# Performance work log

Hardware: AMD Instinct MI355X
Metric: run time of the kernel (lower is better)

Reference implementation:

```python
import jax, jax.numpy as jnp
import numpy as np

B, L, LA, LL = 256, 512, 8, 64
V, D, P, HOPS = 100000, 300, 3, 3


def setup_inputs() -> dict:
    key = jax.random.key(0)
    ks = jax.random.split(key, 18)
    sc = 0.05
    return {
        "text":   jax.random.randint(ks[0], (B, L),  0, V),
        "aspect": jax.random.randint(ks[1], (B, LA), 0, V),
        "left":   jax.random.randint(ks[2], (B, LL), 0, V),
        # pretrained embedding table
        "embed": jax.random.normal(ks[3], (V, D), jnp.float32) * 0.1,
        # all Linear weights stored as [in, out] (y = x @ W + b)
        "Wx": jax.random.normal(ks[4], (D, D), jnp.float32) * sc,   # x_linear (no bias)
        "Ws": jax.random.normal(ks[5], (D, D), jnp.float32) * sc,   # s_linear (no bias)
        "Wk": jax.random.normal(ks[6], (D, D), jnp.float32) * sc,   # attention w_k
        "bk": jnp.zeros((D,), jnp.float32),
        "Wq": jax.random.normal(ks[7], (D, D), jnp.float32) * sc,   # attention w_q
        "bq": jnp.zeros((D,), jnp.float32),
        "w_mlp": jax.random.normal(ks[8], (2 * D,), jnp.float32) * sc,  # attention mlp score vector
        "Wproj": jax.random.normal(ks[9], (D, D), jnp.float32) * sc,    # attention proj
        "bproj": jnp.zeros((D,), jnp.float32),
        "Wm": jax.random.normal(ks[10], (D, D), jnp.float32) * sc,  # mlp
        "bm": jnp.zeros((D,), jnp.float32),
        "Wd": jax.random.normal(ks[11], (D, P), jnp.float32) * sc,  # dense
        "bd": jnp.zeros((P,), jnp.float32),
    }


def _forward(text, aspect, left, embed, Wx, Ws, Wk, bk, Wq, bq, w_mlp,
             Wproj, bproj, Wm, bm, Wd, bd):
    f32 = jnp.float32
    left_len = (left != 0).sum(-1)    # (B,)
    mem_len = (text != 0).sum(-1)     # (B,)
    asp_len = (aspect != 0).sum(-1)   # (B,)
    mem_len_f = mem_len.astype(f32)

    # aspect mean-pooled query (sum over all positions / nonzero count, as in torch code)
    asp_e = embed[aspect].sum(1) / asp_len.astype(f32)[:, None]   # (B, D)
    x = asp_e[:, None, :]                                         # (B, 1, D)

    memory = embed[text]                                          # (B, L, D)
    v_s = (memory.sum(1) / mem_len_f[:, None])[:, None, :]        # (B, 1, D)

    # SqueezeEmbedding (zero padding) + vectorized locationed_memory decay
    idx = jnp.arange(L, dtype=f32)[None, :]                       # (1, L)
    start = (left_len - asp_len).astype(f32)[:, None]             # aspect_start
    end = left_len.astype(f32)[:, None]                           # aspect_end
    l = jnp.where(idx < start, start - idx,
                  jnp.where(idx <= end, 0.0, idx - end))          # (B, L)
    w = 1.0 - l / mem_len_f[:, None]
    w = jnp.where(idx < mem_len_f[:, None], w, 0.0)               # zero padded positions
    memory = memory * w[:, :, None]                               # (B, L, D)

    for _ in range(HOPS):
        x = x @ Wx                                                # (B, 1, D)
        s = v_s @ Ws                                              # computed but unused (faithful)
        # Attention(score_function='mlp', n_head=1, hidden=D)
        kx = memory @ Wk + bk                                     # (B, L, D)
        qx = x @ Wq + bq                                          # (B, 1, D)
        # tanh(cat(kx, qx) @ w_mlp) == tanh(kx@w1 + qx@w2)
        score = jnp.tanh(kx @ w_mlp[:D] + qx @ w_mlp[D:])         # (B, L)
        score = jax.nn.softmax(score, axis=-1)
        v_ts = jnp.einsum('bl,bld->bd', score, kx)[:, None, :]    # (B, 1, D)
        v_ts = v_ts @ Wproj + bproj

    v_ns = (v_ts + v_s).reshape(text.shape[0], -1)                # (B, D)
    v_ms = jnp.tanh(v_ns @ Wm + bm)
    out = jax.nn.softmax(v_ms @ Wd + bd, axis=-1)                 # (B, P)
    return out


def reference(text, aspect, left, embed, Wx, Ws, Wk, bk, Wq, bq, w_mlp,
              Wproj, bproj, Wm, bm, Wd, bd):
    return _forward(text, aspect, left, embed, Wx, Ws, Wk, bk, Wq, bq,
                    w_mlp, Wproj, bproj, Wm, bm, Wd, bd)
```

## Files before the change

kernel.cpp:

```cpp
#include <hip/hip_runtime.h>
#include <math.h>

#define WS_KV   0
#define WS_C0   300
#define WS_C1   301
#define WS_H0   304
#define WS_H1   640
#define WS_ROW  2048
#define WS_ACC  4096
#define WS_VSP  311296
#define WS_SCAL 618496

__device__ __forceinline__ float wred(float v) {
#pragma unroll
    for (int off = 32; off > 0; off >>= 1) v += __shfl_xor(v, off);
    return v;
}

__device__ __forceinline__ float ftanh(float z) {
    float t = __expf(2.f * z);
    return (t - 1.f) / (t + 1.f);
}

__global__ __launch_bounds__(64) void k_prep(
    const float* __restrict__ Wk, const float* __restrict__ bk,
    const float* __restrict__ Wq, const float* __restrict__ bq,
    const float* __restrict__ wmlp, float* __restrict__ ws)
{
    const int lane = threadIdx.x;
    const int j = blockIdx.x;
    const float* u  = wmlp;
    const float* u2 = wmlp + 300;
    if (j < 300) {
        float pk = 0.f, pq = 0.f;
#pragma unroll
        for (int m = 0; m < 5; ++m) {
            int idx = lane + 64 * m;
            if (idx < 300) {
                pk += Wk[j * 300 + idx] * u[idx];
                pq += Wq[j * 300 + idx] * u2[idx];
            }
        }
        pk = wred(pk); pq = wred(pq);
        if (lane == 0) { ws[WS_KV + j] = pk; ws[WS_H0 + j] = pq; }
    } else if (j == 300) {
        float p = 0.f;
#pragma unroll
        for (int m = 0; m < 5; ++m) { int idx = lane + 64 * m; if (idx < 300) p += bk[idx] * u[idx]; }
        p = wred(p);
        if (lane == 0) ws[WS_C0] = p;
    } else {
        float p = 0.f;
#pragma unroll
        for (int m = 0; m < 5; ++m) { int idx = lane + 64 * m; if (idx < 300) p += bq[idx] * u2[idx]; }
        p = wred(p);
        if (lane == 0) ws[WS_C1] = p;
    }
}

__global__ __launch_bounds__(64) void k_hop(
    const float* __restrict__ Wx, const float* __restrict__ src,
    float* __restrict__ dst)
{
    const int lane = threadIdx.x;
    const int j = blockIdx.x;
    float p = 0.f;
#pragma unroll
    for (int m = 0; m < 5; ++m) {
        int idx = lane + 64 * m;
        if (idx < 300) p += Wx[j * 300 + idx] * src[idx];
    }
    p = wred(p);
    if (lane == 0) dst[j] = p;
}

__global__ __launch_bounds__(512) void k_row(
    const int* __restrict__ text, const int* __restrict__ aspect,
    const int* __restrict__ left, const float* __restrict__ embed,
    float* __restrict__ ws)
{
    const int b = blockIdx.x;
    const int t = threadIdx.x, wv = t >> 6, lane = t & 63;

    __shared__ int   atoks[8];
    __shared__ int   cntW[8];
    __shared__ float qp[5];
    __shared__ int   lCnt, aCnt;

    const int tk = text[b * 512 + t];
    {
        unsigned long long m = __ballot(tk != 0);
        if (lane == 0) cntW[wv] = __popcll(m);
    }
    if (wv == 0) {
        unsigned long long m = __ballot(left[b * 64 + lane] != 0);
        if (lane == 0) lCnt = __popcll(m);
    }
    if (wv == 1) {
        int ak = (lane < 8) ? aspect[b * 8 + lane] : 0;
        if (lane < 8) atoks[lane] = ak;
        unsigned long long m = __ballot(lane < 8 && ak != 0);
        if (lane == 0) aCnt = __popcll(m);
    }
    __syncthreads();

    if (wv < 5) {
        float v = 0.f;
        if (t < 300) {
            float s = 0.f;
#pragma unroll
            for (int a = 0; a < 8; ++a) s += embed[(size_t)atoks[a] * 300 + t];
            v = s * ws[WS_H1 + t];
        }
        v = wred(v);
        if (lane == 0) qp[wv] = v;
    }
    __syncthreads();

    if (t == 0) {
        int ml = 0;
#pragma unroll
        for (int w = 0; w < 8; ++w) ml += cntW[w];
        float q = (qp[0] + qp[1] + qp[2] + qp[3] + qp[4]) / (float)aCnt
                + ws[WS_C0] + ws[WS_C1];
        ws[WS_ROW + b * 4 + 0] = (float)ml;
        ws[WS_ROW + b * 4 + 1] = (float)(lCnt - aCnt);
        ws[WS_ROW + b * 4 + 2] = (float)lCnt;
        ws[WS_ROW + b * 4 + 3] = q;
    }
}

__global__ __launch_bounds__(512, 2) void k_main(
    const int* __restrict__ text, const float* __restrict__ embed,
    float* __restrict__ ws)
{
    const int bid = blockIdx.x;
    const int b = bid >> 2, quarter = bid & 3;
    const int t = threadIdx.x, wv = t >> 6, lane = t & 63;

    __shared__ int   toksS[128];
    __shared__ __align__(16) float accW[8 * 300];
    __shared__ __align__(16) float vsW[8 * 300];
    __shared__ float denomW[8], sc[4];

    if (t < 128) toksS[t] = text[b * 512 + quarter * 128 + t];
    if (t >= 128 && t < 132) sc[t - 128] = ws[WS_ROW + b * 4 + (t - 128)];
    __syncthreads();
    const float mem_len_f = sc[0], startf = sc[1], endf = sc[2], qb = sc[3];
    const float inv_ml = 1.f / mem_len_f;

    const float4* kv4  = (const float4*)(ws + WS_KV);
    const float4* emb4 = (const float4*)embed;
    const bool hasB = (lane < 11);
    const float4 kva = kv4[lane];
    const float4 kvb = hasB ? kv4[64 + lane] : make_float4(0.f, 0.f, 0.f, 0.f);
    const float4 fz = make_float4(0.f, 0.f, 0.f, 0.f);

    float4 accA = fz, accB = fz, vsA = fz, vsB = fz;
    float denom = 0.f;
    const float posbase = (float)(quarter * 128);

    for (int it = 0; it < 4; ++it) {
        const int base = wv * 16 + 4 * it;
        int rr[4];
#pragma unroll
        for (int k = 0; k < 4; ++k) rr[k] = toksS[base + k] * 75;
        float4 A[4], Bv[4];
#pragma unroll
        for (int k = 0; k < 4; ++k) A[k] = emb4[rr[k] + lane];
#pragma unroll
        for (int k = 0; k < 4; ++k) Bv[k] = hasB ? emb4[rr[k] + 64 + lane] : fz;

        float pd[4];
#pragma unroll
        for (int k = 0; k < 4; ++k)
            pd[k] = A[k].x*kva.x + A[k].y*kva.y + A[k].z*kva.z + A[k].w*kva.w
                  + Bv[k].x*kvb.x + Bv[k].y*kvb.y + Bv[k].z*kvb.z + Bv[k].w*kvb.w;
#pragma unroll
        for (int off = 32; off > 0; off >>= 1) {
#pragma unroll
            for (int k = 0; k < 4; ++k) pd[k] += __shfl_xor(pd[k], off);
        }

#pragma unroll
        for (int k = 0; k < 4; ++k) {
            const float f = posbase + (float)(base + k);
            float lv = (f < startf) ? (startf - f) : ((f <= endf) ? 0.f : (f - endf));
            float wgt = 1.f - lv * inv_ml;
            wgt = (f < mem_len_f) ? wgt : 0.f;
            const float p = __expf(ftanh(wgt * pd[k] + qb));
            const float pw = p * wgt;
            accA.x += pw * A[k].x;  accA.y += pw * A[k].y;
            accA.z += pw * A[k].z;  accA.w += pw * A[k].w;
            accB.x += pw * Bv[k].x; accB.y += pw * Bv[k].y;
            accB.z += pw * Bv[k].z; accB.w += pw * Bv[k].w;
            vsA.x += A[k].x;  vsA.y += A[k].y;  vsA.z += A[k].z;  vsA.w += A[k].w;
            vsB.x += Bv[k].x; vsB.y += Bv[k].y; vsB.z += Bv[k].z; vsB.w += Bv[k].w;
            denom += p;
        }
    }

    *(float4*)&accW[wv * 300 + 4 * lane] = accA;
    *(float4*)&vsW [wv * 300 + 4 * lane] = vsA;
    if (hasB) {
        *(float4*)&accW[wv * 300 + 256 + 4 * lane] = accB;
        *(float4*)&vsW [wv * 300 + 256 + 4 * lane] = vsB;
    }
    if (lane == 0) denomW[wv] = denom;
    __syncthreads();

    if (t < 300) {
        float ds = 0.f;
#pragma unroll
        for (int w = 0; w < 8; ++w) ds += denomW[w];
        float ms = 0.f, vs = 0.f;
#pragma unroll
        for (int w = 0; w < 8; ++w) { ms += accW[w * 300 + t]; vs += vsW[w * 300 + t]; }
        ws[WS_ACC + bid * 300 + t] = ms;
        ws[WS_VSP + bid * 300 + t] = vs;
        if (t == 0) { ws[WS_SCAL + bid * 2] = ds; ws[WS_SCAL + bid * 2 + 1] = mem_len_f; }
    }
}

__global__ __launch_bounds__(960) void k_tail(
    const float* __restrict__ Wk, const float* __restrict__ bk,
    const float* __restrict__ Wproj, const float* __restrict__ bproj,
    const float* __restrict__ Wm, const float* __restrict__ bm,
    const float* __restrict__ Wd, const float* __restrict__ bd,
    float* __restrict__ out, const float* __restrict__ ws)
{
    const int t = threadIdx.x;
    const int b = blockIdx.x;
    const int seg = t / 320, j = t - seg * 320;

    __shared__ float A[300], T[300], VSs[300], part[900], vms[300], lg[3];

    if (t < 300) {
        const int p0 = (b * 4) * 300 + t;
        float a = ws[WS_ACC + p0] + ws[WS_ACC + p0 + 300]
                + ws[WS_ACC + p0 + 600] + ws[WS_ACC + p0 + 900];
        float v = ws[WS_VSP + p0] + ws[WS_VSP + p0 + 300]
                + ws[WS_VSP + p0 + 600] + ws[WS_VSP + p0 + 900];
        const int s0 = b * 8;
        float d  = ws[WS_SCAL + s0] + ws[WS_SCAL + s0 + 2]
                 + ws[WS_SCAL + s0 + 4] + ws[WS_SCAL + s0 + 6];
        float ml = ws[WS_SCAL + s0 + 1];
        A[t]   = a / d;
        VSs[t] = v / ml;
    }
    __syncthreads();

    if (j < 300) {
        const int k0 = seg * 100;
        float acc = 0.f;
#pragma unroll 10
        for (int i = 0; i < 100; ++i) acc += A[k0 + i] * Wk[(k0 + i) * 300 + j];
        part[seg * 300 + j] = acc;
    }
    __syncthreads();
    if (t < 300) T[t] = part[t] + part[300 + t] + part[600 + t] + bk[t];
    __syncthreads();

    if (j < 300) {
        const int k0 = seg * 100;
        float acc = 0.f;
#pragma unroll 10
        for (int i = 0; i < 100; ++i) acc += T[k0 + i] * Wproj[(k0 + i) * 300 + j];
        part[seg * 300 + j] = acc;
    }
    __syncthreads();
    if (t < 300) A[t] = part[t] + part[300 + t] + part[600 + t] + bproj[t] + VSs[t];
    __syncthreads();

    if (j < 300) {
        const int k0 = seg * 100;
        float acc = 0.f;
#pragma unroll 10
        for (int i = 0; i < 100; ++i) acc += A[k0 + i] * Wm[(k0 + i) * 300 + j];
        part[seg * 300 + j] = acc;
    }
    __syncthreads();
    if (t < 300) vms[t] = tanhf(part[t] + part[300 + t] + part[600 + t] + bm[t]);
    __syncthreads();

    const int wv = t >> 6, lane = t & 63;
    if (wv < 3) {
        float p = 0.f;
#pragma unroll
        for (int k = 0; k < 5; ++k) { int d = lane + 64 * k; if (d < 300) p += vms[d] * Wd[d * 3 + wv]; }
        p = wred(p);
        if (lane == 0) lg[wv] = p + bd[wv];
    }
    __syncthreads();
    if (t == 0) {
        float l0 = lg[0], l1 = lg[1], l2 = lg[2];
        float mx = fmaxf(l0, fmaxf(l1, l2));
        float e0 = expf(l0 - mx), e1 = expf(l1 - mx), e2 = expf(l2 - mx);
        float s = e0 + e1 + e2;
        out[b * 3 + 0] = e0 / s;
        out[b * 3 + 1] = e1 / s;
        out[b * 3 + 2] = e2 / s;
    }
}

extern "C" void kernel_launch(void* const* d_in, const int* in_sizes, int n_in,
                              void* d_out, int out_size, void* d_ws, size_t ws_size,
                              hipStream_t stream)
{
    (void)in_sizes; (void)n_in; (void)out_size; (void)ws_size;
    const int*   text   = (const int*)d_in[0];
    const int*   aspect = (const int*)d_in[1];
    const int*   left   = (const int*)d_in[2];
    const float* embed  = (const float*)d_in[3];
    const float* Wx     = (const float*)d_in[4];
    const float* Wk     = (const float*)d_in[6];
    const float* bk     = (const float*)d_in[7];
    const float* Wq     = (const float*)d_in[8];
    const float* bq     = (const float*)d_in[9];
    const float* wmlp   = (const float*)d_in[10];
    const float* Wproj  = (const float*)d_in[11];
    const float* bproj  = (const float*)d_in[12];
    const float* Wm     = (const float*)d_in[13];
    const float* bm     = (const float*)d_in[14];
    const float* Wd     = (const float*)d_in[15];
    const float* bd     = (const float*)d_in[16];
    float* out = (float*)d_out;
    float* ws  = (float*)d_ws;

    hipLaunchKernelGGL(k_prep, dim3(302), dim3(64), 0, stream, Wk, bk, Wq, bq, wmlp, ws);
    hipLaunchKernelGGL(k_hop, dim3(300), dim3(64), 0, stream, Wx, ws + WS_H0, ws + WS_H1);
    hipLaunchKernelGGL(k_hop, dim3(300), dim3(64), 0, stream, Wx, ws + WS_H1, ws + WS_H0);
    hipLaunchKernelGGL(k_hop, dim3(300), dim3(64), 0, stream, Wx, ws + WS_H0, ws + WS_H1);
    hipLaunchKernelGGL(k_row, dim3(256), dim3(512), 0, stream, text, aspect, left, embed, ws);
    hipLaunchKernelGGL(k_main, dim3(1024), dim3(512), 0, stream, text, embed, ws);
    hipLaunchKernelGGL(k_tail, dim3(256), dim3(960), 0, stream,
                       Wk, bk, Wproj, bproj, Wm, bm, Wd, bd, out, ws);
}
```

Measured before the change: 256.4 us.

## Fuse Wx hop chain into per-row kernel and halve main kernel split

Drops the three k_hop launches, which precomputed a Wx^3 projection of the query vector. Each k_row block now applies the three Wx matvecs to its own aspect vector through shared memory, which removes three tiny dependent launches but adds about 270K FMAs per row, repeated across 256 blocks. k_main now splits each row into 2 blocks instead of 4 (512 blocks, each doing 8 iterations), which shrinks the partial buffers and the reduction in k_tail. The cost is less parallelism in k_main and more weight reads in k_row.

```diff
diff --git a/kernel.cpp b/kernel.cpp
--- a/kernel.cpp
+++ b/kernel.cpp
@@ -4,12 +4,11 @@
 #define WS_KV   0
 #define WS_C0   300
 #define WS_C1   301
-#define WS_H0   304
-#define WS_H1   640
+#define WS_Y    304
 #define WS_ROW  2048
 #define WS_ACC  4096
-#define WS_VSP  311296
-#define WS_SCAL 618496
+#define WS_VSP  161792
+#define WS_SCAL 315392
 
 __device__ __forceinline__ float wred(float v) {
 #pragma unroll
@@ -42,7 +41,7 @@
             }
         }
         pk = wred(pk); pq = wred(pq);
-        if (lane == 0) { ws[WS_KV + j] = pk; ws[WS_H0 + j] = pq; }
+        if (lane == 0) { ws[WS_KV + j] = pk; ws[WS_Y + j] = pq; }
     } else if (j == 300) {
         float p = 0.f;
 #pragma unroll
@@ -58,26 +57,10 @@
     }
 }
 
-__global__ __launch_bounds__(64) void k_hop(
-    const float* __restrict__ Wx, const float* __restrict__ src,
-    float* __restrict__ dst)
-{
-    const int lane = threadIdx.x;
-    const int j = blockIdx.x;
-    float p = 0.f;
-#pragma unroll
-    for (int m = 0; m < 5; ++m) {
-        int idx = lane + 64 * m;
-        if (idx < 300) p += Wx[j * 300 + idx] * src[idx];
-    }
-    p = wred(p);
-    if (lane == 0) dst[j] = p;
-}
-
 __global__ __launch_bounds__(512) void k_row(
     const int* __restrict__ text, const int* __restrict__ aspect,
     const int* __restrict__ left, const float* __restrict__ embed,
-    float* __restrict__ ws)
+    const float* __restrict__ Wx, float* __restrict__ ws)
 {
     const int b = blockIdx.x;
     const int t = threadIdx.x, wv = t >> 6, lane = t & 63;
@@ -85,6 +68,7 @@
     __shared__ int   atoks[8];
     __shared__ int   cntW[8];
     __shared__ float qp[5];
+    __shared__ float xA[300], xB[300];
     __shared__ int   lCnt, aCnt;
 
     const int tk = text[b * 512 + t];
@@ -104,14 +88,30 @@
     }
     __syncthreads();
 
+    if (t < 300) {
+        float s = 0.f;
+#pragma unroll
+        for (int a = 0; a < 8; ++a) s += embed[(size_t)atoks[a] * 300 + t];
+        xA[t] = s / (float)aCnt;
+    }
+    __syncthreads();
+
+#pragma unroll
+    for (int hop = 0; hop < 3; ++hop) {
+        const float* src = (hop & 1) ? xB : xA;
+        float* dst = (hop & 1) ? xA : xB;
+        if (t < 300) {
+            float acc = 0.f;
+#pragma unroll 4
+            for (int i = 0; i < 300; ++i) acc += src[i] * Wx[i * 300 + t];
+            dst[t] = acc;
+        }
+        __syncthreads();
+    }
+
     if (wv < 5) {
         float v = 0.f;
-        if (t < 300) {
-            float s = 0.f;
-#pragma unroll
-            for (int a = 0; a < 8; ++a) s += embed[(size_t)atoks[a] * 300 + t];
-            v = s * ws[WS_H1 + t];
-        }
+        if (t < 300) v = xB[t] * ws[WS_Y + t];
         v = wred(v);
         if (lane == 0) qp[wv] = v;
     }
@@ -121,7 +121,7 @@
         int ml = 0;
 #pragma unroll
         for (int w = 0; w < 8; ++w) ml += cntW[w];
-        float q = (qp[0] + qp[1] + qp[2] + qp[3] + qp[4]) / (float)aCnt
+        float q = qp[0] + qp[1] + qp[2] + qp[3] + qp[4]
                 + ws[WS_C0] + ws[WS_C1];
         ws[WS_ROW + b * 4 + 0] = (float)ml;
         ws[WS_ROW + b * 4 + 1] = (float)(lCnt - aCnt);
@@ -135,16 +135,16 @@
     float* __restrict__ ws)
 {
     const int bid = blockIdx.x;
-    const int b = bid >> 2, quarter = bid & 3;
+    const int b = bid >> 1, half = bid & 1;
     const int t = threadIdx.x, wv = t >> 6, lane = t & 63;
 
-    __shared__ int   toksS[128];
+    __shared__ int   toksS[256];
     __shared__ __align__(16) float accW[8 * 300];
     __shared__ __align__(16) float vsW[8 * 300];
     __shared__ float denomW[8], sc[4];
 
-    if (t < 128) toksS[t] = text[b * 512 + quarter * 128 + t];
-    if (t >= 128 && t < 132) sc[t - 128] = ws[WS_ROW + b * 4 + (t - 128)];
+    if (t < 256) toksS[t] = text[b * 512 + half * 256 + t];
+    if (t >= 256 && t < 260) sc[t - 256] = ws[WS_ROW + b * 4 + (t - 256)];
     __syncthreads();
     const float mem_len_f = sc[0], startf = sc[1], endf = sc[2], qb = sc[3];
     const float inv_ml = 1.f / mem_len_f;
@@ -158,10 +158,10 @@
 
     float4 accA = fz, accB = fz, vsA = fz, vsB = fz;
     float denom = 0.f;
-    const float posbase = (float)(quarter * 128);
-
-    for (int it = 0; it < 4; ++it) {
-        const int base = wv * 16 + 4 * it;
+    const float posbase = (float)(half * 256);
+
+    for (int it = 0; it < 8; ++it) {
+        const int base = wv * 32 + 4 * it;
         int rr[4];
 #pragma unroll
         for (int k = 0; k < 4; ++k) rr[k] = toksS[base + k] * 75;
@@ -236,14 +236,11 @@
     __shared__ float A[300], T[300], VSs[300], part[900], vms[300], lg[3];
 
     if (t < 300) {
-        const int p0 = (b * 4) * 300 + t;
-        float a = ws[WS_ACC + p0] + ws[WS_ACC + p0 + 300]
-                + ws[WS_ACC + p0 + 600] + ws[WS_ACC + p0 + 900];
-        float v = ws[WS_VSP + p0] + ws[WS_VSP + p0 + 300]
-                + ws[WS_VSP + p0 + 600] + ws[WS_VSP + p0 + 900];
-        const int s0 = b * 8;
-        float d  = ws[WS_SCAL + s0] + ws[WS_SCAL + s0 + 2]
-                 + ws[WS_SCAL + s0 + 4] + ws[WS_SCAL + s0 + 6];
+        const int p0 = (b * 2) * 300 + t;
+        float a = ws[WS_ACC + p0] + ws[WS_ACC + p0 + 300];
+        float v = ws[WS_VSP + p0] + ws[WS_VSP + p0 + 300];
+        const int s0 = b * 4;
+        float d  = ws[WS_SCAL + s0] + ws[WS_SCAL + s0 + 2];
         float ml = ws[WS_SCAL + s0 + 1];
         A[t]   = a / d;
         VSs[t] = v / ml;
@@ -328,11 +325,8 @@
     float* ws  = (float*)d_ws;
 
     hipLaunchKernelGGL(k_prep, dim3(302), dim3(64), 0, stream, Wk, bk, Wq, bq, wmlp, ws);
-    hipLaunchKernelGGL(k_hop, dim3(300), dim3(64), 0, stream, Wx, ws + WS_H0, ws + WS_H1);
-    hipLaunchKernelGGL(k_hop, dim3(300), dim3(64), 0, stream, Wx, ws + WS_H1, ws + WS_H0);
-    hipLaunchKernelGGL(k_hop, dim3(300), dim3(64), 0, stream, Wx, ws + WS_H0, ws + WS_H1);
-    hipLaunchKernelGGL(k_row, dim3(256), dim3(512), 0, stream, text, aspect, left, embed, ws);
-    hipLaunchKernelGGL(k_main, dim3(1024), dim3(512), 0, stream, text, embed, ws);
+    hipLaunchKernelGGL(k_row, dim3(256), dim3(512), 0, stream, text, aspect, left, embed, Wx, ws);
+    hipLaunchKernelGGL(k_main, dim3(512), dim3(512), 0, stream, text, embed, ws);
     hipLaunchKernelGGL(k_tail, dim3(256), dim3(960), 0, stream,
                        Wk, bk, Wproj, bproj, Wm, bm, Wd, bd, out, ws);
 }
```

Result: slower. 288.9 us (+12.7%).
